# Kernel optimization log

Measured on AMD Instinct MI355X. Metric: run time of the kernel, lower is better.

The kernel has to match this reference:

```python
import jax, jax.numpy as jnp
import numpy as np

E, S, D_IN, D_LAT, D_HID = 1024, 64, 128, 128, 512
NSTEPS, DT = 8192, 0.01
KL_WEIGHT = 0.01


def setup_inputs() -> dict:
    key = jax.random.key(0)
    ks = jax.random.split(key, 12)
    sd = lambda fan_in: 1.0 / np.sqrt(fan_in)
    return {
        'event_marks': jax.random.normal(ks[0], (E, D_IN), jnp.float32),
        'z_events': jax.random.normal(ks[1], (E, S, D_LAT), jnp.float32),
        'z_traj': jax.random.normal(ks[2], (NSTEPS, S, D_LAT), jnp.float32),
        'times': jnp.arange(NSTEPS + 1, dtype=jnp.float32) * DT,
        'Wp': jax.random.normal(ks[3], (D_IN, D_LAT), jnp.float32) * sd(D_IN),
        'bp': jnp.zeros((D_LAT,), jnp.float32),
        'W1': jax.random.normal(ks[4], (D_LAT, D_HID), jnp.float32) * sd(D_LAT),
        'b1': jnp.zeros((D_HID,), jnp.float32),
        'W2': jax.random.normal(ks[5], (D_HID, 1), jnp.float32) * sd(D_HID),
        'b2': jnp.zeros((1,), jnp.float32),
        'base_intensity': jnp.asarray(0.1, jnp.float32),
        'Wd1': jax.random.normal(ks[6], (D_LAT, D_HID), jnp.float32) * sd(D_LAT),
        'bd1': jnp.zeros((D_HID,), jnp.float32),
        'Wd2': jax.random.normal(ks[7], (D_HID, D_LAT), jnp.float32) * sd(D_HID),
        'bd2': jnp.zeros((D_LAT,), jnp.float32),
    }


def reference(event_marks, z_events, z_traj, times, Wp, bp, W1, b1, W2, b2,
              base_intensity, Wd1, bd1, Wd2, bd2):
    # input projection of marks: [E, D_LAT]
    marks_proj = event_marks @ Wp + bp

    def intensity(z):  # z: [..., D_LAT] -> [...]
        h = jax.nn.relu(z @ W1 + b1)
        s = (h @ W2 + b2)[..., 0]
        return jax.nn.softplus(s + base_intensity)

    # log-intensity at events: sum over events of mean over samples
    lam_ev = intensity(z_events)                      # [E, S]
    log_intensity_sum = jnp.log(lam_ev + 1e-8).mean(axis=1).sum()

    # compensator integral over the trajectory (left Riemann sum)
    lam_traj = intensity(z_traj)                      # [NSTEPS, S]
    dts = jnp.diff(times)                             # [NSTEPS]
    integral = (lam_traj.mean(axis=1) * dts).sum()

    # Gaussian decoder log-prob: mu = MLP(z), unit variance
    h = jax.nn.relu(z_events @ Wd1 + bd1)             # [E, S, D_HID]
    mu = h @ Wd2 + bd2                                # [E, S, D_LAT]
    x = marks_proj[:, None, :]                        # [E, 1, D_LAT]
    log_2pi = jnp.log(jnp.asarray(2.0 * np.pi, jnp.float32))
    log_p = -0.5 * jnp.sum((x - mu) ** 2, axis=-1) - 0.5 * D_LAT * log_2pi  # [E, S]
    recon_loss = log_p.mean(axis=1).sum()

    kl_loss = KL_WEIGHT * jnp.mean(z_traj ** 2)

    elbo = log_intensity_sum - integral + recon_loss - kl_loss
    return -elbo
```

## Files before the change

kernel.cpp:

```cpp
#include <hip/hip_runtime.h>

typedef __attribute__((ext_vector_type(4))) float f32x4;
typedef __attribute__((ext_vector_type(8))) __bf16 bf16x8;
typedef __attribute__((ext_vector_type(4))) __bf16 bf16x4;

#define LOG_2PI 1.8378770664093453f

__device__ __forceinline__ float softplus_f(float x) {
  return fmaxf(x, 0.f) + log1pf(expf(-fabsf(x)));
}

__device__ __forceinline__ void barrier_lds_only() {
  asm volatile("s_waitcnt lgkmcnt(0)\n\ts_barrier" ::: "memory");
}

__global__ void prep_kernel(const float* __restrict__ em,
                            const float* __restrict__ Wp,
                            const float* __restrict__ bp,
                            float* __restrict__ mp,
                            float* __restrict__ accs) {
  const int b = blockIdx.x;
  if (b == 1024) {
    if (threadIdx.x < 8) accs[threadIdx.x] = 0.f;
    return;
  }
  const int d = threadIdx.x;
  float s = bp[d];
  const float* emr = em + b * 128;
#pragma unroll 4
  for (int k = 0; k < 128; ++k) s += emr[k] * Wp[k * 128 + d];
  mp[b * 128 + d] = s;
}

__global__ __launch_bounds__(512, 2) void intensity5_kernel(
    const float* __restrict__ z_traj, const float* __restrict__ z_ev,
    const float* __restrict__ W1, const float* __restrict__ b1,
    const float* __restrict__ W2, const float* __restrict__ b2,
    const float* __restrict__ base_i, const float* __restrict__ times,
    float* __restrict__ accs) {
  __shared__ __align__(16) __bf16 zbuf[2][32 * 128];
  __shared__ float s_part[16][32][9];
  __shared__ float red[8];

  const int tid = threadIdx.x;
  const int wid = tid >> 6, lid = tid & 63;
  const int g = lid >> 4, q = lid & 15;
  const int cb = wid * 64;

  const int b = blockIdx.x;
  const bool traj = (b < 1024);
  const float* z = traj ? z_traj : z_ev;
  const int tile0 = (traj ? b : (b - 1024)) * 16;

  bf16x8 bw[4][4];
#pragma unroll
  for (int cf = 0; cf < 4; ++cf) {
    const int col = cb + cf * 16 + q;
#pragma unroll
    for (int kf = 0; kf < 4; ++kf) {
      bf16x8 f;
#pragma unroll
      for (int j = 0; j < 8; ++j) f[j] = (__bf16)W1[(kf * 32 + g * 8 + j) * 512 + col];
      bw[cf][kf] = f;
    }
  }
  f32x4 bv[4], wv[4];
#pragma unroll
  for (int cf = 0; cf < 4; ++cf) {
    const int c0 = cb + cf * 16 + g * 4;
    bv[cf] = *(const f32x4*)&b1[c0];
    wv[cf] = *(const f32x4*)&W2[c0];
  }
  const float sbias = b2[0] + base_i[0];

  const int srow = tid >> 4, sk8 = (tid & 15) * 8;
  const int stg_byte = ((srow * 256 + sk8 * 2) ^ ((srow & 7) << 4));

  float kls = 0.f;

  {
    const float* p = z + (size_t)tile0 * 4096 + tid * 8;
    f32x4 r0 = *(const f32x4*)p, r1 = *(const f32x4*)(p + 4);
    if (traj) {
      kls += r0[0] * r0[0] + r0[1] * r0[1] + r0[2] * r0[2] + r0[3] * r0[3];
      kls += r1[0] * r1[0] + r1[1] * r1[1] + r1[2] * r1[2] + r1[3] * r1[3];
    }
    bf16x8 v;
#pragma unroll
    for (int j = 0; j < 4; ++j) { v[j] = (__bf16)r0[j]; v[4 + j] = (__bf16)r1[j]; }
    *(bf16x8*)((char*)zbuf[0] + stg_byte) = v;
  }
  f32x4 rA0, rA1, rB0, rB1, rC0, rC1;
  { const float* p = z + (size_t)(tile0 + 1) * 4096 + tid * 8; rA0 = *(const f32x4*)p; rA1 = *(const f32x4*)(p + 4); }
  { const float* p = z + (size_t)(tile0 + 2) * 4096 + tid * 8; rB0 = *(const f32x4*)p; rB1 = *(const f32x4*)(p + 4); }
  { const float* p = z + (size_t)(tile0 + 3) * 4096 + tid * 8; rC0 = *(const f32x4*)p; rC1 = *(const f32x4*)(p + 4); }
  barrier_lds_only();

#define BODY(T, R0, R1, DO_STAGE, DO_ISSUE)                                        \
  do {                                                                             \
    f32x4 acc[2][4] = {};                                                          \
    char* zc = (char*)zbuf[(T) & 1];                                               \
    _Pragma("unroll") for (int kf = 0; kf < 4; ++kf) {                             \
      _Pragma("unroll") for (int rf = 0; rf < 2; ++rf) {                           \
        const int row = rf * 16 + q;                                               \
        bf16x8 a = *(const bf16x8*)(zc + ((row * 256 + kf * 64 + g * 16) ^ ((row & 7) << 4))); \
        _Pragma("unroll") for (int cf = 0; cf < 4; ++cf)                           \
          acc[rf][cf] = __builtin_amdgcn_mfma_f32_16x16x32_bf16(bw[cf][kf], a, acc[rf][cf], 0, 0, 0); \
      }                                                                            \
    }                                                                              \
    if (DO_STAGE) {                                                                \
      if (traj) {                                                                  \
        kls += R0[0] * R0[0] + R0[1] * R0[1] + R0[2] * R0[2] + R0[3] * R0[3];      \
        kls += R1[0] * R1[0] + R1[1] * R1[1] + R1[2] * R1[2] + R1[3] * R1[3];      \
      }                                                                            \
      bf16x8 v;                                                                    \
      _Pragma("unroll") for (int j = 0; j < 4; ++j) { v[j] = (__bf16)R0[j]; v[4 + j] = (__bf16)R1[j]; } \
      *(bf16x8*)((char*)zbuf[((T) + 1) & 1] + stg_byte) = v;                       \
      if (DO_ISSUE) {                                                              \
        const float* p = z + (size_t)(tile0 + (T) + 4) * 4096 + tid * 8;           \
        R0 = *(const f32x4*)p; R1 = *(const f32x4*)(p + 4);                        \
      }                                                                            \
    }                                                                              \
    _Pragma("unroll") for (int rf = 0; rf < 2; ++rf) {                             \
      float partial = 0.f;                                                         \
      _Pragma("unroll") for (int cf = 0; cf < 4; ++cf) {                           \
        _Pragma("unroll") for (int i = 0; i < 4; ++i)                              \
          partial += fmaxf(acc[rf][cf][i] + bv[cf][i], 0.f) * wv[cf][i];           \
      }                                                                            \
      partial += __shfl_xor(partial, 16);                                          \
      partial += __shfl_xor(partial, 32);                                          \
      if (lid < 16) s_part[(T)][rf * 16 + lid][wid] = partial;                     \
    }                                                                              \
    barrier_lds_only();                                                            \
  } while (0)

  int t = 0;
#pragma unroll 1
  for (int it = 0; it < 5; ++it) {
    BODY(t, rA0, rA1, true, (t + 4 <= 15)); ++t;
    BODY(t, rB0, rB1, true, (t + 4 <= 15)); ++t;
    BODY(t, rC0, rC1, true, (t + 4 <= 15)); ++t;
  }
  BODY(t, rA0, rA1, false, false);
#undef BODY

  __syncthreads();
  float local;
  {
    const int tt = tid >> 5, r = tid & 31;
    float s = sbias;
#pragma unroll
    for (int w = 0; w < 8; ++w) s += s_part[tt][r][w];
    const float lam = softplus_f(s);
    if (traj) {
      const int R = (tile0 + tt) * 32 + r;
      const int ts = R >> 6;
      local = lam * (times[ts + 1] - times[ts]) * (1.f / 64.f);
    } else {
      local = logf(lam + 1e-8f) * (1.f / 64.f);
    }
  }
#pragma unroll
  for (int m = 32; m >= 1; m >>= 1) local += __shfl_xor(local, m);
  if (lid == 0) red[wid] = local;
  __syncthreads();
  if (tid == 0) {
    float s = 0.f;
#pragma unroll
    for (int w = 0; w < 8; ++w) s += red[w];
    atomicAdd(traj ? &accs[0] : &accs[1], s);
  }
  if (traj) {
    __syncthreads();
#pragma unroll
    for (int m = 32; m >= 1; m >>= 1) kls += __shfl_xor(kls, m);
    if (lid == 0) red[wid] = kls;
    __syncthreads();
    if (tid == 0) {
      float s = 0.f;
#pragma unroll
      for (int w = 0; w < 8; ++w) s += red[w];
      atomicAdd(&accs[3], s);
    }
  }
}

__global__ __launch_bounds__(512, 2) void decoder2_kernel(
    const float* __restrict__ z,
    const float* __restrict__ Wd1, const float* __restrict__ bd1,
    const float* __restrict__ Wd2, const float* __restrict__ bd2,
    const float* __restrict__ mp, float* __restrict__ recon_acc) {
  __shared__ __align__(16) __bf16 zbuf[2][32 * 128];
  __shared__ __align__(16) __bf16 hbuf[32 * 512];
  __shared__ float s_part[32][9];
  __shared__ float red[8];

  const int tid = threadIdx.x;
  const int wid = tid >> 6, lid = tid & 63;
  const int g = lid >> 4, q = lid & 15;
  const int cb = wid * 64;
  const int tile0 = blockIdx.x * 8;

  bf16x8 bw1[4][4];
  f32x4 bd1v[4];
#pragma unroll
  for (int cf = 0; cf < 4; ++cf) {
    const int col = cb + cf * 16 + q;
#pragma unroll
    for (int i = 0; i < 4; ++i) bd1v[cf][i] = bd1[cb + cf * 16 + g * 4 + i];
#pragma unroll
    for (int kf = 0; kf < 4; ++kf) {
      bf16x8 f;
#pragma unroll
      for (int j = 0; j < 8; ++j) f[j] = (__bf16)Wd1[(kf * 32 + g * 8 + j) * 512 + col];
      bw1[cf][kf] = f;
    }
  }
  const int dimf = wid * 16 + q;
  bf16x8 bw2[16];
#pragma unroll
  for (int kf2 = 0; kf2 < 16; ++kf2) {
    bf16x8 f;
#pragma unroll
    for (int j = 0; j < 8; ++j) f[j] = (__bf16)Wd2[(kf2 * 32 + g * 8 + j) * 128 + dimf];
    bw2[kf2] = f;
  }
  f32x4 bd2v;
#pragma unroll
  for (int i = 0; i < 4; ++i) bd2v[i] = bd2[wid * 16 + g * 4 + i];

  const int srow = tid >> 4, sk8 = (tid & 15) * 8;
  const int stg_byte = ((srow * 256 + sk8 * 2) ^ ((srow & 7) << 4));
  char* hb = (char*)hbuf;

  float local = 0.f;

  {
    const float* p = z + (size_t)tile0 * 4096 + tid * 8;
    f32x4 r0 = *(const f32x4*)p, r1 = *(const f32x4*)(p + 4);
    bf16x8 v;
#pragma unroll
    for (int j = 0; j < 4; ++j) { v[j] = (__bf16)r0[j]; v[4 + j] = (__bf16)r1[j]; }
    *(bf16x8*)((char*)zbuf[0] + stg_byte) = v;
  }
  f32x4 rA0, rA1, rB0, rB1;
  { const float* p = z + (size_t)(tile0 + 1) * 4096 + tid * 8; rA0 = *(const f32x4*)p; rA1 = *(const f32x4*)(p + 4); }
  { const float* p = z + (size_t)(tile0 + 2) * 4096 + tid * 8; rB0 = *(const f32x4*)p; rB1 = *(const f32x4*)(p + 4); }
  barrier_lds_only();

#define DBODY(T, ZC, RR0, RR1)                                                     \
  do {                                                                             \
    f32x4 acc1[2][4] = {};                                                         \
    char* zc = (char*)zbuf[ZC];                                                    \
    _Pragma("unroll") for (int kf = 0; kf < 4; ++kf) {                             \
      _Pragma("unroll") for (int rf = 0; rf < 2; ++rf) {                           \
        const int row = rf * 16 + q;                                               \
        bf16x8 a = *(const bf16x8*)(zc + ((row * 256 + kf * 64 + g * 16) ^ ((row & 7) << 4))); \
        _Pragma("unroll") for (int cf = 0; cf < 4; ++cf)                           \
          acc1[rf][cf] = __builtin_amdgcn_mfma_f32_16x16x32_bf16(bw1[cf][kf], a, acc1[rf][cf], 0, 0, 0); \
      }                                                                            \
    }                                                                              \
    {                                                                              \
      bf16x8 v;                                                                    \
      _Pragma("unroll") for (int j = 0; j < 4; ++j) { v[j] = (__bf16)RR0[j]; v[4 + j] = (__bf16)RR1[j]; } \
      *(bf16x8*)((char*)zbuf[(ZC) ^ 1] + stg_byte) = v;                            \
    }                                                                              \
    {                                                                              \
      int tl = (T) + 3; if (tl > 7) tl = 7;                                        \
      const float* p = z + (size_t)(tile0 + tl) * 4096 + tid * 8;                  \
      RR0 = *(const f32x4*)p; RR1 = *(const f32x4*)(p + 4);                        \
    }                                                                              \
    _Pragma("unroll") for (int rf = 0; rf < 2; ++rf) {                             \
      const int row = rf * 16 + q;                                                 \
      _Pragma("unroll") for (int cf = 0; cf < 4; ++cf) {                           \
        bf16x4 hv;                                                                 \
        _Pragma("unroll") for (int i = 0; i < 4; ++i)                              \
          hv[i] = (__bf16)fmaxf(acc1[rf][cf][i] + bd1v[cf][i], 0.f);               \
        const int byt = ((row * 1024 + (cb + cf * 16 + g * 4) * 2) ^ ((row & 7) << 4)); \
        *(bf16x4*)(hb + byt) = hv;                                                 \
      }                                                                            \
    }                                                                              \
    barrier_lds_only();                                                            \
    f32x4 acc2[2] = {};                                                            \
    _Pragma("unroll") for (int kf2 = 0; kf2 < 16; ++kf2) {                         \
      _Pragma("unroll") for (int rf2 = 0; rf2 < 2; ++rf2) {                        \
        const int row = rf2 * 16 + q;                                              \
        bf16x8 a = *(const bf16x8*)(hb + ((row * 1024 + kf2 * 64 + g * 16) ^ ((row & 7) << 4))); \
        acc2[rf2] = __builtin_amdgcn_mfma_f32_16x16x32_bf16(bw2[kf2], a, acc2[rf2], 0, 0, 0); \
      }                                                                            \
    }                                                                              \
    const int e = (tile0 + (T)) >> 1;                                              \
    _Pragma("unroll") for (int rf2 = 0; rf2 < 2; ++rf2) {                          \
      float partial = 0.f;                                                         \
      _Pragma("unroll") for (int i = 0; i < 4; ++i) {                              \
        const float xv = mp[e * 128 + wid * 16 + g * 4 + i];                       \
        const float d = xv - (acc2[rf2][i] + bd2v[i]);                             \
        partial += d * d;                                                          \
      }                                                                            \
      partial += __shfl_xor(partial, 16);                                          \
      partial += __shfl_xor(partial, 32);                                          \
      if (lid < 16) s_part[rf2 * 16 + lid][wid] = partial;                         \
    }                                                                              \
    barrier_lds_only();                                                            \
    if (tid < 32) {                                                                \
      float t2 = 0.f;                                                              \
      _Pragma("unroll") for (int w = 0; w < 8; ++w) t2 += s_part[tid][w];          \
      local += (-0.5f * t2 - 0.5f * 128.f * LOG_2PI) * (1.f / 64.f);               \
    }                                                                              \
  } while (0)

#pragma unroll 1
  for (int t = 0; t < 8; t += 2) {
    DBODY(t, 0, rA0, rA1);
    DBODY(t + 1, 1, rB0, rB1);
  }
#undef DBODY

  if (wid == 0) {
#pragma unroll
    for (int m = 16; m >= 1; m >>= 1) local += __shfl_xor(local, m);
    if (lid == 0) atomicAdd(recon_acc, local);
  }
}

__global__ void finalize_kernel(const float* __restrict__ accs, float* __restrict__ out) {
  const float kl = 0.01f * (accs[3] / 67108864.f);
  const float elbo = accs[1] - accs[0] + accs[2] - kl;
  out[0] = -elbo;
}

extern "C" void kernel_launch(void* const* d_in, const int* in_sizes, int n_in,
                              void* d_out, int out_size, void* d_ws, size_t ws_size,
                              hipStream_t stream) {
  const float* event_marks = (const float*)d_in[0];
  const float* z_events = (const float*)d_in[1];
  const float* z_traj = (const float*)d_in[2];
  const float* times = (const float*)d_in[3];
  const float* Wp = (const float*)d_in[4];
  const float* bp = (const float*)d_in[5];
  const float* W1 = (const float*)d_in[6];
  const float* b1 = (const float*)d_in[7];
  const float* W2 = (const float*)d_in[8];
  const float* b2 = (const float*)d_in[9];
  const float* base_i = (const float*)d_in[10];
  const float* Wd1 = (const float*)d_in[11];
  const float* bd1 = (const float*)d_in[12];
  const float* Wd2 = (const float*)d_in[13];
  const float* bd2 = (const float*)d_in[14];

  float* mp = (float*)d_ws;
  float* accs = (float*)((char*)d_ws + 1024 * 128 * 4);

  prep_kernel<<<1025, 128, 0, stream>>>(event_marks, Wp, bp, mp, accs);
  intensity5_kernel<<<1152, 512, 0, stream>>>(z_traj, z_events, W1, b1, W2, b2,
                                              base_i, times, accs);
  decoder2_kernel<<<256, 512, 0, stream>>>(z_events, Wd1, bd1, Wd2, bd2, mp,
                                           &accs[2]);
  finalize_kernel<<<1, 1, 0, stream>>>(accs, (float*)d_out);
}
```

Baseline: 183.5 us.

## Stream z tiles into LDS with direct global-to-LDS loads and triple buffering

The intensity kernel's staging path changes. Instead of loading fp32 z into registers, converting to bf16 and writing to LDS, it now uses global_load_lds to copy raw fp32 tiles straight into a swizzled, triple-buffered LDS ring, and converts to bf16 when reading MFMA operands. The goal is to cut register pressure and staging instructions so memory latency overlaps better with compute; b1/W2 also move to LDS and launch bounds rise to 4 blocks per CU. The cost is double the LDS footprint per tile, with the KL sum now computed redundantly by all 8 waves and rescaled by 1/8. The tighter VGPR budget under the new launch bounds may cause spills, since the W1 fragments alone take many registers.

```diff
diff --git a/kernel.cpp b/kernel.cpp
--- a/kernel.cpp
+++ b/kernel.cpp
@@ -12,6 +12,12 @@
 
 __device__ __forceinline__ void barrier_lds_only() {
   asm volatile("s_waitcnt lgkmcnt(0)\n\ts_barrier" ::: "memory");
+}
+
+__device__ __forceinline__ void gload16(const void* g, void* l) {
+  __builtin_amdgcn_global_load_lds(
+      (const __attribute__((address_space(1))) void*)g,
+      (__attribute__((address_space(3))) void*)l, 16, 0, 0);
 }
 
 __global__ void prep_kernel(const float* __restrict__ em,
@@ -32,14 +38,16 @@
   mp[b * 128 + d] = s;
 }
 
-__global__ __launch_bounds__(512, 2) void intensity5_kernel(
+__global__ __launch_bounds__(512, 4) void intensity6_kernel(
     const float* __restrict__ z_traj, const float* __restrict__ z_ev,
     const float* __restrict__ W1, const float* __restrict__ b1,
     const float* __restrict__ W2, const float* __restrict__ b2,
     const float* __restrict__ base_i, const float* __restrict__ times,
     float* __restrict__ accs) {
-  __shared__ __align__(16) __bf16 zbuf[2][32 * 128];
+  __shared__ __align__(16) float zb[3][32 * 128];
   __shared__ float s_part[16][32][9];
+  __shared__ __align__(16) float b1L[512];
+  __shared__ __align__(16) float w2L[512];
   __shared__ float red[8];
 
   const int tid = threadIdx.x;
@@ -52,6 +60,9 @@
   const float* z = traj ? z_traj : z_ev;
   const int tile0 = (traj ? b : (b - 1024)) * 16;
 
+  b1L[tid] = b1[tid];
+  w2L[tid] = W2[tid];
+
   bf16x8 bw[4][4];
 #pragma unroll
   for (int cf = 0; cf < 4; ++cf) {
@@ -64,87 +75,87 @@
       bw[cf][kf] = f;
     }
   }
-  f32x4 bv[4], wv[4];
-#pragma unroll
-  for (int cf = 0; cf < 4; ++cf) {
-    const int c0 = cb + cf * 16 + g * 4;
-    bv[cf] = *(const f32x4*)&b1[c0];
-    wv[cf] = *(const f32x4*)&W2[c0];
-  }
   const float sbias = b2[0] + base_i[0];
 
-  const int srow = tid >> 4, sk8 = (tid & 15) * 8;
-  const int stg_byte = ((srow * 256 + sk8 * 2) ^ ((srow & 7) << 4));
+  const int loff0 = wid * 2048 + lid * 16;
+  const int loff1 = loff0 + 1024;
+  const int swz0 = loff0 ^ (((loff0 >> 9) & 7) << 4);
+  const int swz1 = loff1 ^ (((loff1 >> 9) & 7) << 4);
+  const int dst0 = wid * 2048;
+  const int dst1 = wid * 2048 + 1024;
+
+#define STAGE(TT, SB)                                                      \
+  do {                                                                     \
+    const char* gs = (const char*)(z + (size_t)(tile0 + (TT)) * 4096);     \
+    char* lb = (char*)&zb[SB][0];                                          \
+    gload16(gs + swz0, lb + dst0);                                         \
+    gload16(gs + swz1, lb + dst1);                                         \
+  } while (0)
 
   float kls = 0.f;
 
-  {
-    const float* p = z + (size_t)tile0 * 4096 + tid * 8;
-    f32x4 r0 = *(const f32x4*)p, r1 = *(const f32x4*)(p + 4);
-    if (traj) {
-      kls += r0[0] * r0[0] + r0[1] * r0[1] + r0[2] * r0[2] + r0[3] * r0[3];
-      kls += r1[0] * r1[0] + r1[1] * r1[1] + r1[2] * r1[2] + r1[3] * r1[3];
-    }
-    bf16x8 v;
-#pragma unroll
-    for (int j = 0; j < 4; ++j) { v[j] = (__bf16)r0[j]; v[4 + j] = (__bf16)r1[j]; }
-    *(bf16x8*)((char*)zbuf[0] + stg_byte) = v;
-  }
-  f32x4 rA0, rA1, rB0, rB1, rC0, rC1;
-  { const float* p = z + (size_t)(tile0 + 1) * 4096 + tid * 8; rA0 = *(const f32x4*)p; rA1 = *(const f32x4*)(p + 4); }
-  { const float* p = z + (size_t)(tile0 + 2) * 4096 + tid * 8; rB0 = *(const f32x4*)p; rB1 = *(const f32x4*)(p + 4); }
-  { const float* p = z + (size_t)(tile0 + 3) * 4096 + tid * 8; rC0 = *(const f32x4*)p; rC1 = *(const f32x4*)(p + 4); }
-  barrier_lds_only();
-
-#define BODY(T, R0, R1, DO_STAGE, DO_ISSUE)                                        \
+#define COMPUTE(T, CUR)                                                            \
   do {                                                                             \
-    f32x4 acc[2][4] = {};                                                          \
-    char* zc = (char*)zbuf[(T) & 1];                                               \
-    _Pragma("unroll") for (int kf = 0; kf < 4; ++kf) {                             \
-      _Pragma("unroll") for (int rf = 0; rf < 2; ++rf) {                           \
-        const int row = rf * 16 + q;                                               \
-        bf16x8 a = *(const bf16x8*)(zc + ((row * 256 + kf * 64 + g * 16) ^ ((row & 7) << 4))); \
+    const char* zc = (const char*)&zb[CUR][0];                                     \
+    _Pragma("unroll") for (int rf = 0; rf < 2; ++rf) {                             \
+      const int row = rf * 16 + q;                                                 \
+      const int rowb = row * 512;                                                  \
+      const int sw = (row & 7) << 4;                                               \
+      f32x4 acc[4] = {};                                                           \
+      _Pragma("unroll") for (int kf = 0; kf < 4; ++kf) {                           \
+        const int x0 = kf * 128 + g * 32;                                          \
+        f32x4 a0 = *(const f32x4*)(zc + rowb + (x0 ^ sw));                         \
+        f32x4 a1 = *(const f32x4*)(zc + rowb + ((x0 + 16) ^ sw));                  \
+        if (traj) {                                                                \
+          kls += a0[0] * a0[0] + a0[1] * a0[1] + a0[2] * a0[2] + a0[3] * a0[3];    \
+          kls += a1[0] * a1[0] + a1[1] * a1[1] + a1[2] * a1[2] + a1[3] * a1[3];    \
+        }                                                                          \
+        bf16x8 af;                                                                 \
+        _Pragma("unroll") for (int j = 0; j < 4; ++j) {                            \
+          af[j] = (__bf16)a0[j];                                                   \
+          af[4 + j] = (__bf16)a1[j];                                               \
+        }                                                                          \
         _Pragma("unroll") for (int cf = 0; cf < 4; ++cf)                           \
-          acc[rf][cf] = __builtin_amdgcn_mfma_f32_16x16x32_bf16(bw[cf][kf], a, acc[rf][cf], 0, 0, 0); \
-      }                                                                            \
-    }                                                                              \
-    if (DO_STAGE) {                                                                \
-      if (traj) {                                                                  \
-        kls += R0[0] * R0[0] + R0[1] * R0[1] + R0[2] * R0[2] + R0[3] * R0[3];      \
-        kls += R1[0] * R1[0] + R1[1] * R1[1] + R1[2] * R1[2] + R1[3] * R1[3];      \
-      }                                                                            \
-      bf16x8 v;                                                                    \
-      _Pragma("unroll") for (int j = 0; j < 4; ++j) { v[j] = (__bf16)R0[j]; v[4 + j] = (__bf16)R1[j]; } \
-      *(bf16x8*)((char*)zbuf[((T) + 1) & 1] + stg_byte) = v;                       \
-      if (DO_ISSUE) {                                                              \
-        const float* p = z + (size_t)(tile0 + (T) + 4) * 4096 + tid * 8;           \
-        R0 = *(const f32x4*)p; R1 = *(const f32x4*)(p + 4);                        \
-      }                                                                            \
-    }                                                                              \
-    _Pragma("unroll") for (int rf = 0; rf < 2; ++rf) {                             \
+          acc[cf] = __builtin_amdgcn_mfma_f32_16x16x32_bf16(bw[cf][kf], af, acc[cf], 0, 0, 0); \
+      }                                                                            \
       float partial = 0.f;                                                         \
       _Pragma("unroll") for (int cf = 0; cf < 4; ++cf) {                           \
+        const int c0 = cb + cf * 16 + g * 4;                                       \
+        f32x4 bb = *(const f32x4*)&b1L[c0];                                        \
+        f32x4 ww = *(const f32x4*)&w2L[c0];                                        \
         _Pragma("unroll") for (int i = 0; i < 4; ++i)                              \
-          partial += fmaxf(acc[rf][cf][i] + bv[cf][i], 0.f) * wv[cf][i];           \
+          partial += fmaxf(acc[cf][i] + bb[i], 0.f) * ww[i];                       \
       }                                                                            \
       partial += __shfl_xor(partial, 16);                                          \
       partial += __shfl_xor(partial, 32);                                          \
-      if (lid < 16) s_part[(T)][rf * 16 + lid][wid] = partial;                     \
-    }                                                                              \
-    barrier_lds_only();                                                            \
+      if (lid < 16) s_part[T][rf * 16 + lid][wid] = partial;                       \
+    }                                                                              \
   } while (0)
 
-  int t = 0;
+  STAGE(0, 0);
+  STAGE(1, 1);
+  asm volatile("s_waitcnt vmcnt(2) lgkmcnt(0)\n\ts_barrier" ::: "memory");
+
+  int cur = 0;
 #pragma unroll 1
-  for (int it = 0; it < 5; ++it) {
-    BODY(t, rA0, rA1, true, (t + 4 <= 15)); ++t;
-    BODY(t, rB0, rB1, true, (t + 4 <= 15)); ++t;
-    BODY(t, rC0, rC1, true, (t + 4 <= 15)); ++t;
-  }
-  BODY(t, rA0, rA1, false, false);
-#undef BODY
-
+  for (int t = 0; t < 14; ++t) {
+    int sb = cur + 2;
+    if (sb >= 3) sb -= 3;
+    STAGE(t + 2, sb);
+    COMPUTE(t, cur);
+    asm volatile("s_waitcnt vmcnt(2) lgkmcnt(0)\n\ts_barrier" ::: "memory");
+    ++cur;
+    if (cur >= 3) cur -= 3;
+  }
+  COMPUTE(14, cur);
+  asm volatile("s_waitcnt vmcnt(0) lgkmcnt(0)\n\ts_barrier" ::: "memory");
+  ++cur;
+  if (cur >= 3) cur -= 3;
+  COMPUTE(15, cur);
   __syncthreads();
+#undef COMPUTE
+#undef STAGE
+
   float local;
   {
     const int tt = tid >> 5, r = tid & 31;
@@ -180,7 +191,7 @@
       float s = 0.f;
 #pragma unroll
       for (int w = 0; w < 8; ++w) s += red[w];
-      atomicAdd(&accs[3], s);
+      atomicAdd(&accs[3], s * 0.125f);
     }
   }
 }
@@ -352,7 +363,7 @@
   float* accs = (float*)((char*)d_ws + 1024 * 128 * 4);
 
   prep_kernel<<<1025, 128, 0, stream>>>(event_marks, Wp, bp, mp, accs);
-  intensity5_kernel<<<1152, 512, 0, stream>>>(z_traj, z_events, W1, b1, W2, b2,
+  intensity6_kernel<<<1152, 512, 0, stream>>>(z_traj, z_events, W1, b1, W2, b2,
                                               base_i, times, accs);
   decoder2_kernel<<<256, 512, 0, stream>>>(z_events, Wd1, bd1, Wd2, bd2, mp,
                                            &accs[2]);
```

Result: slower. 206.3 us (+12.4%).

## Restructure intensity kernel: W1 in LDS, per-wave row tiles in registers

Applied to the files above, without the earlier changes.

Rewrites the intensity kernel so that each block stages the full W1 (as bf16) in LDS and each wave independently processes 9 tiles of 32 rows. The z rows are loaded straight into registers as MFMA operands, with the next tile prefetched. Waves loop over all 512 hidden columns and accumulate the W2-weighted ReLU per row, which removes the cross-wave s_part reduction and the per-tile barriers. The grid shrinks to 256 persistent blocks at one block per CU. The costs are 128KB of LDS per block, more LDS reads of W1 per tile, and lower occupancy.

```diff
diff --git a/kernel.cpp b/kernel.cpp
--- a/kernel.cpp
+++ b/kernel.cpp
@@ -32,156 +32,152 @@
   mp[b * 128 + d] = s;
 }
 
-__global__ __launch_bounds__(512, 2) void intensity5_kernel(
+__global__ __launch_bounds__(512, 1) void intensity7_kernel(
     const float* __restrict__ z_traj, const float* __restrict__ z_ev,
     const float* __restrict__ W1, const float* __restrict__ b1,
     const float* __restrict__ W2, const float* __restrict__ b2,
     const float* __restrict__ base_i, const float* __restrict__ times,
     float* __restrict__ accs) {
-  __shared__ __align__(16) __bf16 zbuf[2][32 * 128];
-  __shared__ float s_part[16][32][9];
-  __shared__ float red[8];
+  __shared__ __align__(16) __bf16 w1t[512 * 128];
+  __shared__ __align__(16) float b1L[512];
+  __shared__ __align__(16) float w2L[512];
+  __shared__ float red[8][4];
 
   const int tid = threadIdx.x;
   const int wid = tid >> 6, lid = tid & 63;
   const int g = lid >> 4, q = lid & 15;
-  const int cb = wid * 64;
-
-  const int b = blockIdx.x;
-  const bool traj = (b < 1024);
-  const float* z = traj ? z_traj : z_ev;
-  const int tile0 = (traj ? b : (b - 1024)) * 16;
-
-  bf16x8 bw[4][4];
-#pragma unroll
-  for (int cf = 0; cf < 4; ++cf) {
-    const int col = cb + cf * 16 + q;
-#pragma unroll
-    for (int kf = 0; kf < 4; ++kf) {
-      bf16x8 f;
-#pragma unroll
-      for (int j = 0; j < 8; ++j) f[j] = (__bf16)W1[(kf * 32 + g * 8 + j) * 512 + col];
-      bw[cf][kf] = f;
-    }
-  }
-  f32x4 bv[4], wv[4];
-#pragma unroll
-  for (int cf = 0; cf < 4; ++cf) {
-    const int c0 = cb + cf * 16 + g * 4;
-    bv[cf] = *(const f32x4*)&b1[c0];
-    wv[cf] = *(const f32x4*)&W2[c0];
+
+  const int gw = blockIdx.x * 8 + wid;
+  const int t0 = gw * 9;
+
+  f32x4 rz[2][4][2];
+#define LOADT(TILE)                                                            \
+  do {                                                                         \
+    const float* zp = ((TILE) < 16384)                                         \
+                          ? z_traj + (size_t)(TILE) * 4096                     \
+                          : z_ev + (size_t)((TILE) - 16384) * 4096;            \
+    _Pragma("unroll") for (int s = 0; s < 2; ++s) {                            \
+      _Pragma("unroll") for (int kf = 0; kf < 4; ++kf) {                       \
+        const float* pp = zp + (s * 16 + q) * 128 + kf * 32 + g * 8;           \
+        rz[s][kf][0] = *(const f32x4*)pp;                                      \
+        rz[s][kf][1] = *(const f32x4*)(pp + 4);                                \
+      }                                                                        \
+    }                                                                          \
+  } while (0)
+  LOADT(t0);
+
+  {
+    const float* wcol = W1 + tid;
+    char* wb = (char*)w1t;
+    const int colbase = tid * 256;
+    const int sw = (tid & 7) << 4;
+#pragma unroll 8
+    for (int k = 0; k < 128; k += 2) {
+      float a = wcol[(size_t)k * 512];
+      float c = wcol[(size_t)(k + 1) * 512];
+      union { __bf16 h[2]; unsigned u; } pk;
+      pk.h[0] = (__bf16)a;
+      pk.h[1] = (__bf16)c;
+      *(unsigned*)(wb + (colbase + ((k * 2) ^ sw))) = pk.u;
+    }
+    b1L[tid] = b1[tid];
+    w2L[tid] = W2[tid];
   }
   const float sbias = b2[0] + base_i[0];
-
-  const int srow = tid >> 4, sk8 = (tid & 15) * 8;
-  const int stg_byte = ((srow * 256 + sk8 * 2) ^ ((srow & 7) << 4));
-
-  float kls = 0.f;
-
-  {
-    const float* p = z + (size_t)tile0 * 4096 + tid * 8;
-    f32x4 r0 = *(const f32x4*)p, r1 = *(const f32x4*)(p + 4);
-    if (traj) {
-      kls += r0[0] * r0[0] + r0[1] * r0[1] + r0[2] * r0[2] + r0[3] * r0[3];
-      kls += r1[0] * r1[0] + r1[1] * r1[1] + r1[2] * r1[2] + r1[3] * r1[3];
-    }
-    bf16x8 v;
-#pragma unroll
-    for (int j = 0; j < 4; ++j) { v[j] = (__bf16)r0[j]; v[4 + j] = (__bf16)r1[j]; }
-    *(bf16x8*)((char*)zbuf[0] + stg_byte) = v;
-  }
-  f32x4 rA0, rA1, rB0, rB1, rC0, rC1;
-  { const float* p = z + (size_t)(tile0 + 1) * 4096 + tid * 8; rA0 = *(const f32x4*)p; rA1 = *(const f32x4*)(p + 4); }
-  { const float* p = z + (size_t)(tile0 + 2) * 4096 + tid * 8; rB0 = *(const f32x4*)p; rB1 = *(const f32x4*)(p + 4); }
-  { const float* p = z + (size_t)(tile0 + 3) * 4096 + tid * 8; rC0 = *(const f32x4*)p; rC1 = *(const f32x4*)(p + 4); }
   barrier_lds_only();
 
-#define BODY(T, R0, R1, DO_STAGE, DO_ISSUE)                                        \
-  do {                                                                             \
-    f32x4 acc[2][4] = {};                                                          \
-    char* zc = (char*)zbuf[(T) & 1];                                               \
-    _Pragma("unroll") for (int kf = 0; kf < 4; ++kf) {                             \
-      _Pragma("unroll") for (int rf = 0; rf < 2; ++rf) {                           \
-        const int row = rf * 16 + q;                                               \
-        bf16x8 a = *(const bf16x8*)(zc + ((row * 256 + kf * 64 + g * 16) ^ ((row & 7) << 4))); \
-        _Pragma("unroll") for (int cf = 0; cf < 4; ++cf)                           \
-          acc[rf][cf] = __builtin_amdgcn_mfma_f32_16x16x32_bf16(bw[cf][kf], a, acc[rf][cf], 0, 0, 0); \
-      }                                                                            \
-    }                                                                              \
-    if (DO_STAGE) {                                                                \
-      if (traj) {                                                                  \
-        kls += R0[0] * R0[0] + R0[1] * R0[1] + R0[2] * R0[2] + R0[3] * R0[3];      \
-        kls += R1[0] * R1[0] + R1[1] * R1[1] + R1[2] * R1[2] + R1[3] * R1[3];      \
-      }                                                                            \
-      bf16x8 v;                                                                    \
-      _Pragma("unroll") for (int j = 0; j < 4; ++j) { v[j] = (__bf16)R0[j]; v[4 + j] = (__bf16)R1[j]; } \
-      *(bf16x8*)((char*)zbuf[((T) + 1) & 1] + stg_byte) = v;                       \
-      if (DO_ISSUE) {                                                              \
-        const float* p = z + (size_t)(tile0 + (T) + 4) * 4096 + tid * 8;           \
-        R0 = *(const f32x4*)p; R1 = *(const f32x4*)(p + 4);                        \
-      }                                                                            \
-    }                                                                              \
-    _Pragma("unroll") for (int rf = 0; rf < 2; ++rf) {                             \
-      float partial = 0.f;                                                         \
-      _Pragma("unroll") for (int cf = 0; cf < 4; ++cf) {                           \
-        _Pragma("unroll") for (int i = 0; i < 4; ++i)                              \
-          partial += fmaxf(acc[rf][cf][i] + bv[cf][i], 0.f) * wv[cf][i];           \
-      }                                                                            \
-      partial += __shfl_xor(partial, 16);                                          \
-      partial += __shfl_xor(partial, 32);                                          \
-      if (lid < 16) s_part[(T)][rf * 16 + lid][wid] = partial;                     \
-    }                                                                              \
-    barrier_lds_only();                                                            \
-  } while (0)
-
-  int t = 0;
+  float integral_loc = 0.f, logsum_loc = 0.f, kls = 0.f;
+  const char* wb = (const char*)w1t;
+  const int wsw = (q & 7) << 4;
+
 #pragma unroll 1
-  for (int it = 0; it < 5; ++it) {
-    BODY(t, rA0, rA1, true, (t + 4 <= 15)); ++t;
-    BODY(t, rB0, rB1, true, (t + 4 <= 15)); ++t;
-    BODY(t, rC0, rC1, true, (t + 4 <= 15)); ++t;
-  }
-  BODY(t, rA0, rA1, false, false);
-#undef BODY
-
-  __syncthreads();
-  float local;
-  {
-    const int tt = tid >> 5, r = tid & 31;
-    float s = sbias;
-#pragma unroll
-    for (int w = 0; w < 8; ++w) s += s_part[tt][r][w];
-    const float lam = softplus_f(s);
-    if (traj) {
-      const int R = (tile0 + tt) * 32 + r;
-      const int ts = R >> 6;
-      local = lam * (times[ts + 1] - times[ts]) * (1.f / 64.f);
-    } else {
-      local = logf(lam + 1e-8f) * (1.f / 64.f);
-    }
-  }
-#pragma unroll
-  for (int m = 32; m >= 1; m >>= 1) local += __shfl_xor(local, m);
-  if (lid == 0) red[wid] = local;
+  for (int i = 0; i < 9; ++i) {
+    const int tile = t0 + i;
+    const bool traj_t = (tile < 16384);
+
+    bf16x8 fr[2][4];
+#pragma unroll
+    for (int s = 0; s < 2; ++s) {
+#pragma unroll
+      for (int kf = 0; kf < 4; ++kf) {
+        f32x4 a0 = rz[s][kf][0], a1 = rz[s][kf][1];
+        if (traj_t) {
+          kls += a0[0] * a0[0] + a0[1] * a0[1] + a0[2] * a0[2] + a0[3] * a0[3];
+          kls += a1[0] * a1[0] + a1[1] * a1[1] + a1[2] * a1[2] + a1[3] * a1[3];
+        }
+        bf16x8 f;
+#pragma unroll
+        for (int j = 0; j < 4; ++j) {
+          f[j] = (__bf16)a0[j];
+          f[4 + j] = (__bf16)a1[j];
+        }
+        fr[s][kf] = f;
+      }
+    }
+    if (i < 8) LOADT(tile + 1);
+    __builtin_amdgcn_sched_barrier(0);
+
+    float rowacc0 = 0.f, rowacc1 = 0.f;
+#pragma unroll 4
+    for (int c = 0; c < 32; ++c) {
+      f32x4 a0 = {}, a1 = {};
+#pragma unroll
+      for (int kf = 0; kf < 4; ++kf) {
+        bf16x8 wf = *(const bf16x8*)(wb + c * 4096 + q * 256 +
+                                     ((kf * 64 + g * 16) ^ wsw));
+        a0 = __builtin_amdgcn_mfma_f32_16x16x32_bf16(wf, fr[0][kf], a0, 0, 0, 0);
+        a1 = __builtin_amdgcn_mfma_f32_16x16x32_bf16(wf, fr[1][kf], a1, 0, 0, 0);
+      }
+      f32x4 bb = *(const f32x4*)&b1L[c * 16 + g * 4];
+      f32x4 ww = *(const f32x4*)&w2L[c * 16 + g * 4];
+#pragma unroll
+      for (int ii = 0; ii < 4; ++ii) {
+        rowacc0 += fmaxf(a0[ii] + bb[ii], 0.f) * ww[ii];
+        rowacc1 += fmaxf(a1[ii] + bb[ii], 0.f) * ww[ii];
+      }
+    }
+    rowacc0 += __shfl_xor(rowacc0, 16);
+    rowacc0 += __shfl_xor(rowacc0, 32);
+    rowacc1 += __shfl_xor(rowacc1, 16);
+    rowacc1 += __shfl_xor(rowacc1, 32);
+
+    if (lid < 32) {
+      const float rs = (lid < 16) ? rowacc0 : rowacc1;
+      const float lam = softplus_f(rs + sbias);
+      if (traj_t) {
+        const int R = tile * 32 + lid;
+        const int ts = R >> 6;
+        integral_loc += lam * (times[ts + 1] - times[ts]) * (1.f / 64.f);
+      } else {
+        logsum_loc += logf(lam + 1e-8f) * (1.f / 64.f);
+      }
+    }
+  }
+#undef LOADT
+
+#pragma unroll
+  for (int m = 32; m >= 1; m >>= 1) {
+    integral_loc += __shfl_xor(integral_loc, m);
+    logsum_loc += __shfl_xor(logsum_loc, m);
+    kls += __shfl_xor(kls, m);
+  }
+  if (lid == 0) {
+    red[wid][0] = integral_loc;
+    red[wid][1] = logsum_loc;
+    red[wid][2] = kls;
+  }
   __syncthreads();
   if (tid == 0) {
-    float s = 0.f;
-#pragma unroll
-    for (int w = 0; w < 8; ++w) s += red[w];
-    atomicAdd(traj ? &accs[0] : &accs[1], s);
-  }
-  if (traj) {
-    __syncthreads();
-#pragma unroll
-    for (int m = 32; m >= 1; m >>= 1) kls += __shfl_xor(kls, m);
-    if (lid == 0) red[wid] = kls;
-    __syncthreads();
-    if (tid == 0) {
-      float s = 0.f;
-#pragma unroll
-      for (int w = 0; w < 8; ++w) s += red[w];
-      atomicAdd(&accs[3], s);
-    }
+    float I = 0.f, L = 0.f, K = 0.f;
+#pragma unroll
+    for (int w = 0; w < 8; ++w) {
+      I += red[w][0];
+      L += red[w][1];
+      K += red[w][2];
+    }
+    atomicAdd(&accs[0], I);
+    atomicAdd(&accs[1], L);
+    atomicAdd(&accs[3], K);
   }
 }
 
@@ -352,8 +348,8 @@
   float* accs = (float*)((char*)d_ws + 1024 * 128 * 4);
 
   prep_kernel<<<1025, 128, 0, stream>>>(event_marks, Wp, bp, mp, accs);
-  intensity5_kernel<<<1152, 512, 0, stream>>>(z_traj, z_events, W1, b1, W2, b2,
-                                              base_i, times, accs);
+  intensity7_kernel<<<256, 512, 0, stream>>>(z_traj, z_events, W1, b1, W2, b2,
+                                             base_i, times, accs);
   decoder2_kernel<<<256, 512, 0, stream>>>(z_events, Wd1, bd1, Wd2, bd2, mp,
                                            &accs[2]);
   finalize_kernel<<<1, 1, 0, stream>>>(accs, (float*)d_out);
```

New measurement: 151.6 us. -17.4%, faster.
